# Kernel tuning notes

Measured on AMD Instinct MI355X. Metric: run time of the kernel, lower is better.

Reference implementation:

```python
import jax, jax.numpy as jnp
import numpy as np

B_NW, N, DIM, NH, DH, HID, NW, WH = 2048, 64, 512, 16, 32, 384, 64, 8
EPS = 1e-12  # F.normalize eps

def _rel_coords_log(wh, ww):
    # torch.cartesian_prod order: i (rows) outer, j (cols) inner
    ii, jj = np.meshgrid(np.arange(wh), np.arange(ww), indexing='ij')
    coords = np.stack([ii.ravel(), jj.ravel()], axis=-1).astype(np.float32)  # [N,2]
    rel = coords[:, None, :] - coords[None, :, :]                            # [N,N,2]
    return (np.sign(rel) * np.log1p(np.abs(rel))).astype(np.float32)

def setup_inputs() -> dict:
    key = jax.random.key(0)
    ks = jax.random.split(key, 9)
    s = 0.02
    inner = NH * DH
    return {
        'x': jax.random.normal(ks[0], (B_NW, N, DIM), jnp.float32),
        'mask': jax.random.normal(ks[1], (NW, N, N), jnp.float32),
        'w_qkv': jax.random.normal(ks[2], (DIM, 3 * inner), jnp.float32) * s,
        'tau': jnp.ones((1, NH, 1, 1), jnp.float32),
        'mlp_w1': jax.random.normal(ks[3], (2, HID), jnp.float32) * s,
        'mlp_b1': jnp.zeros((HID,), jnp.float32),
        'mlp_w2': jax.random.normal(ks[4], (HID, NH), jnp.float32) * s,
        'mlp_b2': jnp.zeros((NH,), jnp.float32),
        'w_out': jax.random.normal(ks[5], (inner, DIM), jnp.float32) * s,
        'b_out': jnp.zeros((DIM,), jnp.float32),
        'rel_log': jnp.asarray(_rel_coords_log(WH, WH)),
    }

def reference(x, mask, w_qkv, tau, mlp_w1, mlp_b1, mlp_w2, mlp_b2, w_out, b_out, rel_log):
    b, n, _ = x.shape
    qkv = x @ w_qkv                                   # [b, n, 3*nh*dh]
    qkv = qkv.reshape(b, n, 3, NH, DH)
    q, k, v = (jnp.transpose(qkv[:, :, i], (0, 2, 1, 3)) for i in range(3))  # [b, nh, n, dh]
    # cosine attention: L2-normalize q and k along head dim
    q = q / jnp.maximum(jnp.linalg.norm(q, axis=-1, keepdims=True), EPS)
    k = k / jnp.maximum(jnp.linalg.norm(k, axis=-1, keepdims=True), EPS)
    sim = jnp.einsum('bhid,bhjd->bhij', q, k) * tau   # learned temperature
    # relative position bias via meta MLP: [N,N,2] -> [N,N,nh]
    bias = jax.nn.relu(rel_log @ mlp_w1 + mlp_b1) @ mlp_w2 + mlp_b2
    sim = sim + jnp.transpose(bias, (2, 0, 1))[None]  # [1, nh, N, N]
    nw = mask.shape[0]
    sim = sim.reshape(b // nw, nw, NH, n, n) + mask[None, :, None]
    sim = sim.reshape(b, NH, n, n)
    attn = jax.nn.softmax(sim, axis=-1)
    out = jnp.einsum('bhij,bhjd->bhid', attn, v)
    out = jnp.transpose(out, (0, 2, 1, 3)).reshape(b, n, NH * DH)
    return out @ w_out + b_out
```

## Files before the change

### kernel.cpp

```cpp
#include <hip/hip_runtime.h>
#include <hip/hip_bf16.h>


typedef __bf16 bf16;
typedef __bf16 v4bf __attribute__((ext_vector_type(4)));
typedef __bf16 v8bf __attribute__((ext_vector_type(8)));
typedef float  v4f  __attribute__((ext_vector_type(4)));

#define AS1 __attribute__((address_space(1)))
#define AS3 __attribute__((address_space(3)))

__device__ __forceinline__ int swzA(int o) { return o ^ (((o >> 10) & 7) << 4); }

__global__ void convert_w_kernel(const float* __restrict__ wqkv, const float* __restrict__ wout,
                                 bf16* __restrict__ Wt, bf16* __restrict__ WoT) {
    int idx = blockIdx.x * 256 + threadIdx.x;
    Wt[idx] = (bf16)wqkv[(idx & 511) * 1536 + (idx >> 9)];
    if (idx < 262144) WoT[idx] = (bf16)wout[(idx & 511) * 512 + (idx >> 9)];
}

__global__ void bias_kernel(const float* __restrict__ rel_log, const float* __restrict__ w1,
                            const float* __restrict__ b1, const float* __restrict__ w2,
                            const float* __restrict__ b2, float* __restrict__ bias) {
    int p = blockIdx.x * 256 + threadIdx.x;
    float ra = rel_log[p * 2 + 0];
    float rb = rel_log[p * 2 + 1];
    float acc[16];
    #pragma unroll
    for (int t = 0; t < 16; ++t) acc[t] = 0.f;
    for (int kk = 0; kk < 384; ++kk) {
        float hv = fmaxf(ra * w1[kk] + rb * w1[384 + kk] + b1[kk], 0.f);
        #pragma unroll
        for (int t = 0; t < 16; ++t) acc[t] += hv * w2[kk * 16 + t];
    }
    #pragma unroll
    for (int t = 0; t < 16; ++t) bias[t * 4096 + p] = acc[t] + b2[t];
}

__global__ void comb_kernel(const float* __restrict__ bias, const float* __restrict__ mask,
                            float* __restrict__ comb) {
    int idx = blockIdx.x * 256 + threadIdx.x;
    int t = idx & 4095, wh = idx >> 12;
    int w = wh >> 4, h = wh & 15;
    int ji = t >> 8, rem = t & 255;
    int j = ji >> 2, i = ji & 3;
    int q16 = rem >> 2, r = t & 3;
    int lq = q16 >> 4, lm = q16 & 15;
    int p = (i * 16 + lm) * 64 + j * 16 + lq * 4 + r;
    comb[idx] = bias[h * 4096 + p] + mask[w * 4096 + p];
}

__global__ __launch_bounds__(512) void qkv_fused_kernel(
    const float* __restrict__ x,
    const bf16* __restrict__ Wt,
    bf16* __restrict__ q_ws, bf16* __restrict__ k_ws, bf16* __restrict__ v_ws)
{
    __shared__ alignas(16) char Albuf[131072];
    __shared__ alignas(16) char Blbuf[2][16384];
    const int mb = blockIdx.x;
    const int t = threadIdx.x;
    const int wv = t >> 6, lane = t & 63, lq = lane >> 4, lm = lane & 15;
    const int wr = wv >> 2, wc = wv & 3;

    auto stageB = [&](int buf, int pass, int kt) {
        const char* bBase = (const char*)Wt + (size_t)(pass * 256) * 1024;
        #pragma unroll
        for (int p = 0; p < 2; ++p) {
            int o = p * 8192 + t * 16;
            __builtin_amdgcn_global_load_lds(
                (const AS1 void*)(bBase + (size_t)(o >> 6) * 1024 + kt * 64 + (o & 63)),
                (AS3 void*)(&Blbuf[buf][0] + o), 16, 0, 0);
        }
    };

    stageB(0, 0, 0);

    {
        const char* xbase = (const char*)x + (size_t)mb * 128 * 2048;
        #pragma unroll
        for (int p = 0; p < 16; ++p) {
            int o = p * 8192 + t * 16;
            const float4* src = (const float4*)(xbase + (size_t)o * 2);
            float4 f0 = src[0], f1 = src[1];
            v8bf a = { (bf16)f0.x, (bf16)f0.y, (bf16)f0.z, (bf16)f0.w,
                       (bf16)f1.x, (bf16)f1.y, (bf16)f1.z, (bf16)f1.w };
            *(v8bf*)(&Albuf[swzA(o)]) = a;
        }
    }
    __syncthreads();

    int abase[4], boff[4];
    #pragma unroll
    for (int i = 0; i < 4; ++i) {
        int row = wr * 64 + i * 16 + lm;
        abase[i] = (row * 1024 + lq * 16) ^ ((row & 7) << 4);
        boff[i] = (wc * 64 + i * 16 + lm) * 64 + lq * 16;
    }

    v4f acc[4][4];
    #pragma unroll
    for (int i = 0; i < 4; ++i)
        #pragma unroll
        for (int j = 0; j < 4; ++j) acc[i][j] = v4f{0.f, 0.f, 0.f, 0.f};

    const int bw = mb * 2 + wr;

    #pragma unroll 1
    for (int ph = 0; ph < 96; ++ph) {
        const int pass = ph >> 4, kt = ph & 15;
        if (ph < 95) {
            const int nph = ph + 1;
            stageB(nph & 1, nph >> 4, nph & 15);
            asm volatile("s_waitcnt vmcnt(2)" ::: "memory");
        } else {
            asm volatile("s_waitcnt vmcnt(0)" ::: "memory");
        }
        __builtin_amdgcn_s_barrier();
        __builtin_amdgcn_sched_barrier(0);
        const char* Bb = &Blbuf[ph & 1][0];
        v8bf af[4], bfj[4];
        #pragma unroll
        for (int i = 0; i < 4; ++i) af[i] = *(const v8bf*)(&Albuf[abase[i] ^ (kt << 6)]);
        #pragma unroll
        for (int j = 0; j < 4; ++j) bfj[j] = *(const v8bf*)(Bb + boff[j]);
        #pragma unroll
        for (int i = 0; i < 4; ++i)
            #pragma unroll
            for (int j = 0; j < 4; ++j)
                acc[i][j] = __builtin_amdgcn_mfma_f32_16x16x32_bf16(af[i], bfj[j], acc[i][j], 0, 0, 0);
        __builtin_amdgcn_s_barrier();

        if (kt == 15) {
            const int hbase = (pass & 1) * 8 + wc * 2;
            if (pass < 4) {
                bf16* dst = (pass < 2) ? q_ws : k_ws;
                #pragma unroll
                for (int tpair = 0; tpair < 2; ++tpair) {
                    const int h = hbase + tpair;
                    #pragma unroll
                    for (int i = 0; i < 4; ++i)
                        #pragma unroll
                        for (int r = 0; r < 4; ++r) {
                            int n = i * 16 + lq * 4 + r;
                            size_t base = ((size_t)(bw * 16 + h) * 64 + n) * 32;
                            dst[base + lm]      = (bf16)acc[i][2 * tpair][r];
                            dst[base + 16 + lm] = (bf16)acc[i][2 * tpair + 1][r];
                        }
                }
            } else {
                #pragma unroll
                for (int j = 0; j < 4; ++j) {
                    const int h = hbase + (j >> 1);
                    const int dh = (j & 1) * 16 + lm;
                    #pragma unroll
                    for (int i = 0; i < 4; ++i) {
                        v4bf pv = { (bf16)acc[i][j][0], (bf16)acc[i][j][1],
                                    (bf16)acc[i][j][2], (bf16)acc[i][j][3] };
                        *(v4bf*)(v_ws + ((size_t)(bw * 16 + h) * 32 + dh) * 64 + i * 16 + lq * 4) = pv;
                    }
                }
            }
            #pragma unroll
            for (int i = 0; i < 4; ++i)
                #pragma unroll
                for (int j = 0; j < 4; ++j) acc[i][j] = v4f{0.f, 0.f, 0.f, 0.f};
        }
    }
}

__global__ __launch_bounds__(512) void attn_proj_kernel(
    const bf16* __restrict__ q_ws,
    const bf16* __restrict__ k_ws,
    const bf16* __restrict__ v_ws,
    const float* __restrict__ comb,
    const float* __restrict__ tau,
    const bf16* __restrict__ WoT,
    const float* __restrict__ b_out,
    int wofs,
    float* __restrict__ out)
{
    __shared__ alignas(16) bf16 AO[64 * 520];
    __shared__ alignas(16) bf16 P_all[8][64 * 72];
    const int b = blockIdx.x;
    const int tid = threadIdx.x;
    const int wv = tid >> 6, lane = tid & 63, lq = lane >> 4, lm = lane & 15;
    const v4f z4 = {0.f, 0.f, 0.f, 0.f};
    bf16* P = P_all[wv];

    #pragma unroll 1
    for (int hh = 0; hh < 2; ++hh) {
        const int h = wv * 2 + hh;
        const size_t qk_base = (size_t)(b * 16 + h) * 64 * 32;
        const float* comb_hw = comb + ((size_t)(((wofs + b) & 63) * 16 + h)) * 4096
                                    + (lq * 16 + lm) * 4;
        const float tau_h = tau[h];

        v8bf qf[4], kf[4];
        #pragma unroll
        for (int i = 0; i < 4; ++i)
            qf[i] = *(const v8bf*)(q_ws + qk_base + (i * 16 + lm) * 32 + lq * 8);
        #pragma unroll
        for (int j = 0; j < 4; ++j)
            kf[j] = *(const v8bf*)(k_ws + qk_base + (j * 16 + lm) * 32 + lq * 8);

        #pragma unroll
        for (int i = 0; i < 4; ++i) {
            float a = 0.f;
            #pragma unroll
            for (int e = 0; e < 8; ++e) { float f = (float)qf[i][e]; a = fmaf(f, f, a); }
            a += __shfl_xor(a, 16); a += __shfl_xor(a, 32);
            float sc = tau_h / fmaxf(sqrtf(a), 1e-12f);
            #pragma unroll
            for (int e = 0; e < 8; ++e) qf[i][e] = (bf16)((float)qf[i][e] * sc);
        }
        #pragma unroll
        for (int j = 0; j < 4; ++j) {
            float a = 0.f;
            #pragma unroll
            for (int e = 0; e < 8; ++e) { float f = (float)kf[j][e]; a = fmaf(f, f, a); }
            a += __shfl_xor(a, 16); a += __shfl_xor(a, 32);
            float sc = 1.0f / fmaxf(sqrtf(a), 1e-12f);
            #pragma unroll
            for (int e = 0; e < 8; ++e) kf[j][e] = (bf16)((float)kf[j][e] * sc);
        }

        v4f st[4][4];
        #pragma unroll
        for (int j = 0; j < 4; ++j)
            #pragma unroll
            for (int i = 0; i < 4; ++i)
                st[j][i] = __builtin_amdgcn_mfma_f32_16x16x32_bf16(kf[j], qf[i], z4, 0, 0, 0);

        #pragma unroll
        for (int j = 0; j < 4; ++j)
            #pragma unroll
            for (int i = 0; i < 4; ++i) {
                float4 cv = *(const float4*)(comb_hw + (j * 4 + i) * 256);
                st[j][i][0] += cv.x; st[j][i][1] += cv.y;
                st[j][i][2] += cv.z; st[j][i][3] += cv.w;
            }

        #pragma unroll
        for (int i = 0; i < 4; ++i) {
            float mx = st[0][i][0];
            #pragma unroll
            for (int j = 0; j < 4; ++j)
                #pragma unroll
                for (int r = 0; r < 4; ++r) mx = fmaxf(mx, st[j][i][r]);
            mx = fmaxf(mx, __shfl_xor(mx, 16));
            mx = fmaxf(mx, __shfl_xor(mx, 32));
            float sm = 0.f;
            #pragma unroll
            for (int j = 0; j < 4; ++j)
                #pragma unroll
                for (int r = 0; r < 4; ++r) {
                    float e = __expf(st[j][i][r] - mx);
                    st[j][i][r] = e; sm += e;
                }
            sm += __shfl_xor(sm, 16); sm += __shfl_xor(sm, 32);
            float rcp = 1.0f / sm;
            #pragma unroll
            for (int j = 0; j < 4; ++j) {
                v4bf pv = { (bf16)(st[j][i][0] * rcp), (bf16)(st[j][i][1] * rcp),
                            (bf16)(st[j][i][2] * rcp), (bf16)(st[j][i][3] * rcp) };
                *(v4bf*)(P + (i * 16 + lm) * 72 + j * 16 + lq * 4) = pv;
            }
        }

        const size_t v_base = (size_t)(b * 16 + h) * 32 * 64;
        v4f o[4][2];
        #pragma unroll
        for (int i = 0; i < 4; ++i)
            #pragma unroll
            for (int nt = 0; nt < 2; ++nt) o[i][nt] = z4;
        #pragma unroll
        for (int kk = 0; kk < 2; ++kk) {
            v8bf vf[2], pf[4];
            #pragma unroll
            for (int nt = 0; nt < 2; ++nt)
                vf[nt] = *(const v8bf*)(v_ws + v_base + (nt * 16 + lm) * 64 + kk * 32 + lq * 8);
            #pragma unroll
            for (int i = 0; i < 4; ++i)
                pf[i] = *(const v8bf*)(P + (i * 16 + lm) * 72 + kk * 32 + lq * 8);
            #pragma unroll
            for (int i = 0; i < 4; ++i)
                #pragma unroll
                for (int nt = 0; nt < 2; ++nt)
                    o[i][nt] = __builtin_amdgcn_mfma_f32_16x16x32_bf16(pf[i], vf[nt], o[i][nt], 0, 0, 0);
        }
        #pragma unroll
        for (int i = 0; i < 4; ++i)
            #pragma unroll
            for (int nt = 0; nt < 2; ++nt)
                #pragma unroll
                for (int r = 0; r < 4; ++r)
                    AO[(i * 16 + lq * 4 + r) * 520 + h * 32 + nt * 16 + lm] = (bf16)o[i][nt][r];
    }

    __syncthreads();

    v4f acc[4][4];
    #pragma unroll
    for (int i = 0; i < 4; ++i)
        #pragma unroll
        for (int j = 0; j < 4; ++j) acc[i][j] = v4f{0.f, 0.f, 0.f, 0.f};

    #pragma unroll 2
    for (int kc = 0; kc < 16; ++kc) {
        v8bf af[4], bfj[4];
        #pragma unroll
        for (int j = 0; j < 4; ++j)
            bfj[j] = *(const v8bf*)(WoT + (size_t)(wv * 64 + j * 16 + lm) * 512 + kc * 32 + lq * 8);
        #pragma unroll
        for (int i = 0; i < 4; ++i)
            af[i] = *(const v8bf*)(AO + (i * 16 + lm) * 520 + kc * 32 + lq * 8);
        #pragma unroll
        for (int i = 0; i < 4; ++i)
            #pragma unroll
            for (int j = 0; j < 4; ++j)
                acc[i][j] = __builtin_amdgcn_mfma_f32_16x16x32_bf16(af[i], bfj[j], acc[i][j], 0, 0, 0);
    }

    #pragma unroll
    for (int j = 0; j < 4; ++j) {
        const int col = wv * 64 + j * 16 + lm;
        const float bo = b_out[col];
        #pragma unroll
        for (int i = 0; i < 4; ++i)
            #pragma unroll
            for (int r = 0; r < 4; ++r)
                out[(size_t)(b * 64 + i * 16 + lq * 4 + r) * 512 + col] = acc[i][j][r] + bo;
    }
}

extern "C" void kernel_launch(void* const* d_in, const int* in_sizes, int n_in,
                              void* d_out, int out_size, void* d_ws, size_t ws_size,
                              hipStream_t stream) {
    (void)in_sizes; (void)n_in; (void)out_size;
    const float* x       = (const float*)d_in[0];
    const float* mask    = (const float*)d_in[1];
    const float* w_qkv   = (const float*)d_in[2];
    const float* tau     = (const float*)d_in[3];
    const float* mlp_w1  = (const float*)d_in[4];
    const float* mlp_b1  = (const float*)d_in[5];
    const float* mlp_w2  = (const float*)d_in[6];
    const float* mlp_b2  = (const float*)d_in[7];
    const float* w_out   = (const float*)d_in[8];
    const float* b_out   = (const float*)d_in[9];
    const float* rel_log = (const float*)d_in[10];
    float* out = (float*)d_out;

    char* ws = (char*)d_ws;
    bf16*  Wt     = (bf16*)(ws);
    bf16*  WoT    = (bf16*)(ws + 1572864);
    float* bias   = (float*)(ws + 2097152);
    float* comb   = (float*)(ws + 2359296);
    char*  qkv_base = ws + 19136512;

    size_t avail = (ws_size > 19136512ULL) ? ws_size - 19136512ULL : 0;
    int W = 2048;
    while (W > 128 && (size_t)W * 196608ULL > avail) W >>= 1;
    const size_t qkbuf = (size_t)W * 65536;
    bf16* qb = (bf16*)qkv_base;
    bf16* kb = (bf16*)(qkv_base + qkbuf);
    bf16* vb = (bf16*)(qkv_base + 2 * qkbuf);

    convert_w_kernel<<<3072, 256, 0, stream>>>(w_qkv, w_out, Wt, WoT);
    bias_kernel<<<16, 256, 0, stream>>>(rel_log, mlp_w1, mlp_b1, mlp_w2, mlp_b2, bias);
    comb_kernel<<<16384, 256, 0, stream>>>(bias, mask, comb);

    const int nchunk = 2048 / W;
    for (int c = 0; c < nchunk; ++c) {
        const float* xc = x + (size_t)c * W * 64 * 512;
        qkv_fused_kernel<<<W / 2, 512, 0, stream>>>(xc, Wt, qb, kb, vb);
        attn_proj_kernel<<<W, 512, 0, stream>>>(qb, kb, vb, comb, tau, WoT, b_out,
                                                c * W, out + (size_t)c * W * 64 * 512);
    }
}
```

Baseline: 736.7 us.

## Software-pipeline per-head global loads across the two heads in attention kernel

Unrolls the two-head loop into explicit lambdas. All global loads (q, k, comb bias/mask, v) for the first head are issued up front, the second head's q/k are prefetched early, and its comb/v loads are issued right after the first head's QK MFMAs. This hides global memory latency behind compute. The cost is much higher register pressure (two sets of 16 float4 plus fragments), which may reduce occupancy at 512 threads or cause spills.

```diff
diff --git a/kernel.cpp b/kernel.cpp
--- a/kernel.cpp
+++ b/kernel.cpp
@@ -186,23 +186,34 @@
     const int wv = tid >> 6, lane = tid & 63, lq = lane >> 4, lm = lane & 15;
     const v4f z4 = {0.f, 0.f, 0.f, 0.f};
     bf16* P = P_all[wv];
-
-    #pragma unroll 1
-    for (int hh = 0; hh < 2; ++hh) {
-        const int h = wv * 2 + hh;
+    const int h0 = wv * 2, h1 = wv * 2 + 1;
+
+    auto load_qk = [&](int h, v8bf (&qf)[4], v8bf (&kf)[4]) {
         const size_t qk_base = (size_t)(b * 16 + h) * 64 * 32;
+        #pragma unroll
+        for (int i = 0; i < 4; ++i)
+            qf[i] = *(const v8bf*)(q_ws + qk_base + (i * 16 + lm) * 32 + lq * 8);
+        #pragma unroll
+        for (int j = 0; j < 4; ++j)
+            kf[j] = *(const v8bf*)(k_ws + qk_base + (j * 16 + lm) * 32 + lq * 8);
+    };
+    auto load_aux = [&](int h, float4 (&cv)[16], v8bf (&vf)[4]) {
         const float* comb_hw = comb + ((size_t)(((wofs + b) & 63) * 16 + h)) * 4096
                                     + (lq * 16 + lm) * 4;
+        #pragma unroll
+        for (int ji = 0; ji < 16; ++ji)
+            cv[ji] = *(const float4*)(comb_hw + ji * 256);
+        const size_t v_base = (size_t)(b * 16 + h) * 32 * 64;
+        #pragma unroll
+        for (int kk = 0; kk < 2; ++kk)
+            #pragma unroll
+            for (int nt = 0; nt < 2; ++nt)
+                vf[kk * 2 + nt] = *(const v8bf*)(v_ws + v_base + (nt * 16 + lm) * 64 + kk * 32 + lq * 8);
+    };
+
+    auto head_compute = [&](int h, v8bf (&qf)[4], v8bf (&kf)[4], float4 (&cv)[16],
+                            v8bf (&vf)[4], auto mid_hook) {
         const float tau_h = tau[h];
-
-        v8bf qf[4], kf[4];
-        #pragma unroll
-        for (int i = 0; i < 4; ++i)
-            qf[i] = *(const v8bf*)(q_ws + qk_base + (i * 16 + lm) * 32 + lq * 8);
-        #pragma unroll
-        for (int j = 0; j < 4; ++j)
-            kf[j] = *(const v8bf*)(k_ws + qk_base + (j * 16 + lm) * 32 + lq * 8);
-
         #pragma unroll
         for (int i = 0; i < 4; ++i) {
             float a = 0.f;
@@ -231,13 +242,14 @@
             for (int i = 0; i < 4; ++i)
                 st[j][i] = __builtin_amdgcn_mfma_f32_16x16x32_bf16(kf[j], qf[i], z4, 0, 0, 0);
 
+        mid_hook();
+
         #pragma unroll
         for (int j = 0; j < 4; ++j)
             #pragma unroll
             for (int i = 0; i < 4; ++i) {
-                float4 cv = *(const float4*)(comb_hw + (j * 4 + i) * 256);
-                st[j][i][0] += cv.x; st[j][i][1] += cv.y;
-                st[j][i][2] += cv.z; st[j][i][3] += cv.w;
+                st[j][i][0] += cv[j * 4 + i].x; st[j][i][1] += cv[j * 4 + i].y;
+                st[j][i][2] += cv[j * 4 + i].z; st[j][i][3] += cv[j * 4 + i].w;
             }
 
         #pragma unroll
@@ -267,7 +279,6 @@
             }
         }
 
-        const size_t v_base = (size_t)(b * 16 + h) * 32 * 64;
         v4f o[4][2];
         #pragma unroll
         for (int i = 0; i < 4; ++i)
@@ -275,10 +286,7 @@
             for (int nt = 0; nt < 2; ++nt) o[i][nt] = z4;
         #pragma unroll
         for (int kk = 0; kk < 2; ++kk) {
-            v8bf vf[2], pf[4];
-            #pragma unroll
-            for (int nt = 0; nt < 2; ++nt)
-                vf[nt] = *(const v8bf*)(v_ws + v_base + (nt * 16 + lm) * 64 + kk * 32 + lq * 8);
+            v8bf pf[4];
             #pragma unroll
             for (int i = 0; i < 4; ++i)
                 pf[i] = *(const v8bf*)(P + (i * 16 + lm) * 72 + kk * 32 + lq * 8);
@@ -286,7 +294,7 @@
             for (int i = 0; i < 4; ++i)
                 #pragma unroll
                 for (int nt = 0; nt < 2; ++nt)
-                    o[i][nt] = __builtin_amdgcn_mfma_f32_16x16x32_bf16(pf[i], vf[nt], o[i][nt], 0, 0, 0);
+                    o[i][nt] = __builtin_amdgcn_mfma_f32_16x16x32_bf16(pf[i], vf[kk * 2 + nt], o[i][nt], 0, 0, 0);
         }
         #pragma unroll
         for (int i = 0; i < 4; ++i)
@@ -295,7 +303,15 @@
                 #pragma unroll
                 for (int r = 0; r < 4; ++r)
                     AO[(i * 16 + lq * 4 + r) * 520 + h * 32 + nt * 16 + lm] = (bf16)o[i][nt][r];
-    }
+    };
+
+    v8bf qfA[4], kfA[4], qfB[4], kfB[4], vfA[4], vfB[4];
+    float4 cvA[16], cvB[16];
+    load_qk(h0, qfA, kfA);
+    load_aux(h0, cvA, vfA);
+    load_qk(h1, qfB, kfB);
+    head_compute(h0, qfA, kfA, cvA, vfA, [&] { load_aux(h1, cvB, vfB); });
+    head_compute(h1, qfB, kfB, cvB, vfB, [] {});
 
     __syncthreads();
 
```

Measured after the change: 745.4 us. About the same (+1.2%).

## Restructure QKV GEMM to 64-row tiles reading weights directly from global

Applied to the files above, without the earlier changes.

Each block of the QKV projection now handles one 64-row window instead of two. The weight operand is read straight from global/L2 into registers rather than staged through double-buffered LDS with async loads and barriers, and the launch bounds ask for more blocks per CU. Each wave owns a 64-column slice of each Q/K/V pass, so the per-phase barriers go away and LDS use drops to 64KB for higher occupancy. The cost is that each weight slice is reused across only 64 rows, which doubles weight traffic, and the B fragment loads are uncoalesced global reads that may expose latency.

```diff
diff --git a/kernel.cpp b/kernel.cpp
--- a/kernel.cpp
+++ b/kernel.cpp
@@ -6,9 +6,6 @@
 typedef __bf16 v4bf __attribute__((ext_vector_type(4)));
 typedef __bf16 v8bf __attribute__((ext_vector_type(8)));
 typedef float  v4f  __attribute__((ext_vector_type(4)));
-
-#define AS1 __attribute__((address_space(1)))
-#define AS3 __attribute__((address_space(3)))
 
 __device__ __forceinline__ int swzA(int o) { return o ^ (((o >> 10) & 7) << 4); }
 
@@ -50,35 +47,20 @@
     comb[idx] = bias[h * 4096 + p] + mask[w * 4096 + p];
 }
 
-__global__ __launch_bounds__(512) void qkv_fused_kernel(
+__global__ __launch_bounds__(512, 4) void qkv_fused_kernel(
     const float* __restrict__ x,
     const bf16* __restrict__ Wt,
     bf16* __restrict__ q_ws, bf16* __restrict__ k_ws, bf16* __restrict__ v_ws)
 {
-    __shared__ alignas(16) char Albuf[131072];
-    __shared__ alignas(16) char Blbuf[2][16384];
+    __shared__ alignas(16) char Albuf[65536];
     const int mb = blockIdx.x;
     const int t = threadIdx.x;
     const int wv = t >> 6, lane = t & 63, lq = lane >> 4, lm = lane & 15;
-    const int wr = wv >> 2, wc = wv & 3;
-
-    auto stageB = [&](int buf, int pass, int kt) {
-        const char* bBase = (const char*)Wt + (size_t)(pass * 256) * 1024;
-        #pragma unroll
-        for (int p = 0; p < 2; ++p) {
-            int o = p * 8192 + t * 16;
-            __builtin_amdgcn_global_load_lds(
-                (const AS1 void*)(bBase + (size_t)(o >> 6) * 1024 + kt * 64 + (o & 63)),
-                (AS3 void*)(&Blbuf[buf][0] + o), 16, 0, 0);
-        }
-    };
-
-    stageB(0, 0, 0);
 
     {
-        const char* xbase = (const char*)x + (size_t)mb * 128 * 2048;
-        #pragma unroll
-        for (int p = 0; p < 16; ++p) {
+        const char* xbase = (const char*)x + (size_t)mb * 64 * 2048;
+        #pragma unroll
+        for (int p = 0; p < 8; ++p) {
             int o = p * 8192 + t * 16;
             const float4* src = (const float4*)(xbase + (size_t)o * 2);
             float4 f0 = src[0], f1 = src[1];
@@ -89,81 +71,67 @@
     }
     __syncthreads();
 
-    int abase[4], boff[4];
+    int abase[4];
     #pragma unroll
     for (int i = 0; i < 4; ++i) {
-        int row = wr * 64 + i * 16 + lm;
+        int row = i * 16 + lm;
         abase[i] = (row * 1024 + lq * 16) ^ ((row & 7) << 4);
-        boff[i] = (wc * 64 + i * 16 + lm) * 64 + lq * 16;
-    }
-
-    v4f acc[4][4];
-    #pragma unroll
-    for (int i = 0; i < 4; ++i)
-        #pragma unroll
-        for (int j = 0; j < 4; ++j) acc[i][j] = v4f{0.f, 0.f, 0.f, 0.f};
-
-    const int bw = mb * 2 + wr;
+    }
+
+    const int bw = mb;
 
     #pragma unroll 1
-    for (int ph = 0; ph < 96; ++ph) {
-        const int pass = ph >> 4, kt = ph & 15;
-        if (ph < 95) {
-            const int nph = ph + 1;
-            stageB(nph & 1, nph >> 4, nph & 15);
-            asm volatile("s_waitcnt vmcnt(2)" ::: "memory");
+    for (int pass = 0; pass < 3; ++pass) {
+        const bf16* bBase = Wt + (size_t)(pass * 512 + wv * 64) * 512;
+
+        v4f acc[4][4];
+        #pragma unroll
+        for (int i = 0; i < 4; ++i)
+            #pragma unroll
+            for (int j = 0; j < 4; ++j) acc[i][j] = v4f{0.f, 0.f, 0.f, 0.f};
+
+        #pragma unroll 4
+        for (int kt = 0; kt < 16; ++kt) {
+            v8bf af[4], bfj[4];
+            #pragma unroll
+            for (int j = 0; j < 4; ++j)
+                bfj[j] = *(const v8bf*)(bBase + (size_t)(j * 16 + lm) * 512 + kt * 32 + lq * 8);
+            #pragma unroll
+            for (int i = 0; i < 4; ++i)
+                af[i] = *(const v8bf*)(&Albuf[abase[i] ^ (kt << 6)]);
+            #pragma unroll
+            for (int i = 0; i < 4; ++i)
+                #pragma unroll
+                for (int j = 0; j < 4; ++j)
+                    acc[i][j] = __builtin_amdgcn_mfma_f32_16x16x32_bf16(af[i], bfj[j], acc[i][j], 0, 0, 0);
+        }
+
+        if (pass < 2) {
+            bf16* dst = (pass == 0) ? q_ws : k_ws;
+            #pragma unroll
+            for (int j = 0; j < 4; ++j) {
+                const int h = wv * 2 + (j >> 1);
+                const int dcol = (j & 1) * 16 + lm;
+                #pragma unroll
+                for (int i = 0; i < 4; ++i)
+                    #pragma unroll
+                    for (int r = 0; r < 4; ++r) {
+                        int n = i * 16 + lq * 4 + r;
+                        dst[((size_t)(bw * 16 + h) * 64 + n) * 32 + dcol] = (bf16)acc[i][j][r];
+                    }
+            }
         } else {
-            asm volatile("s_waitcnt vmcnt(0)" ::: "memory");
-        }
-        __builtin_amdgcn_s_barrier();
-        __builtin_amdgcn_sched_barrier(0);
-        const char* Bb = &Blbuf[ph & 1][0];
-        v8bf af[4], bfj[4];
-        #pragma unroll
-        for (int i = 0; i < 4; ++i) af[i] = *(const v8bf*)(&Albuf[abase[i] ^ (kt << 6)]);
-        #pragma unroll
-        for (int j = 0; j < 4; ++j) bfj[j] = *(const v8bf*)(Bb + boff[j]);
-        #pragma unroll
-        for (int i = 0; i < 4; ++i)
-            #pragma unroll
-            for (int j = 0; j < 4; ++j)
-                acc[i][j] = __builtin_amdgcn_mfma_f32_16x16x32_bf16(af[i], bfj[j], acc[i][j], 0, 0, 0);
-        __builtin_amdgcn_s_barrier();
-
-        if (kt == 15) {
-            const int hbase = (pass & 1) * 8 + wc * 2;
-            if (pass < 4) {
-                bf16* dst = (pass < 2) ? q_ws : k_ws;
-                #pragma unroll
-                for (int tpair = 0; tpair < 2; ++tpair) {
-                    const int h = hbase + tpair;
-                    #pragma unroll
-                    for (int i = 0; i < 4; ++i)
-                        #pragma unroll
-                        for (int r = 0; r < 4; ++r) {
-                            int n = i * 16 + lq * 4 + r;
-                            size_t base = ((size_t)(bw * 16 + h) * 64 + n) * 32;
-                            dst[base + lm]      = (bf16)acc[i][2 * tpair][r];
-                            dst[base + 16 + lm] = (bf16)acc[i][2 * tpair + 1][r];
-                        }
-                }
-            } else {
-                #pragma unroll
-                for (int j = 0; j < 4; ++j) {
-                    const int h = hbase + (j >> 1);
-                    const int dh = (j & 1) * 16 + lm;
-                    #pragma unroll
-                    for (int i = 0; i < 4; ++i) {
-                        v4bf pv = { (bf16)acc[i][j][0], (bf16)acc[i][j][1],
-                                    (bf16)acc[i][j][2], (bf16)acc[i][j][3] };
-                        *(v4bf*)(v_ws + ((size_t)(bw * 16 + h) * 32 + dh) * 64 + i * 16 + lq * 4) = pv;
-                    }
+            #pragma unroll
+            for (int j = 0; j < 4; ++j) {
+                const int h = wv * 2 + (j >> 1);
+                const int dh = (j & 1) * 16 + lm;
+                #pragma unroll
+                for (int i = 0; i < 4; ++i) {
+                    v4bf pv = { (bf16)acc[i][j][0], (bf16)acc[i][j][1],
+                                (bf16)acc[i][j][2], (bf16)acc[i][j][3] };
+                    *(v4bf*)(v_ws + ((size_t)(bw * 16 + h) * 32 + dh) * 64 + i * 16 + lq * 4) = pv;
                 }
             }
-            #pragma unroll
-            for (int i = 0; i < 4; ++i)
-                #pragma unroll
-                for (int j = 0; j < 4; ++j) acc[i][j] = v4f{0.f, 0.f, 0.f, 0.f};
         }
     }
 }
@@ -372,7 +340,7 @@
     const int nchunk = 2048 / W;
     for (int c = 0; c < nchunk; ++c) {
         const float* xc = x + (size_t)c * W * 64 * 512;
-        qkv_fused_kernel<<<W / 2, 512, 0, stream>>>(xc, Wt, qb, kb, vb);
+        qkv_fused_kernel<<<W, 512, 0, stream>>>(xc, Wt, qb, kb, vb);
         attn_proj_kernel<<<W, 512, 0, stream>>>(qb, kb, vb, comb, tau, WoT, b_out,
                                                 c * W, out + (size_t)c * W * 64 * 512);
     }
```

After: 783.0 us. +6.3%, slower.
